# Performance work log

Measured on AMD Instinct MI355X. Metric: run time of the kernel, lower is better.

The kernel has to match this reference:

```python
import jax, jax.numpy as jnp
import numpy as np

EPS = 1e-10

def _iou(a, b):
    """IoU for boxes in (cx, cy, w, h) format; a, b: (..., 4)."""
    a_min = a[..., :2] - a[..., 2:] * 0.5
    a_max = a[..., :2] + a[..., 2:] * 0.5
    b_min = b[..., :2] - b[..., 2:] * 0.5
    b_max = b[..., :2] + b[..., 2:] * 0.5
    inter_wh = jnp.clip(jnp.minimum(a_max, b_max) - jnp.maximum(a_min, b_min), 0.0)
    inter = inter_wh[..., 0] * inter_wh[..., 1]
    area_a = a[..., 2] * a[..., 3]
    area_b = b[..., 2] * b[..., 3]
    return inter / (area_a + area_b - inter + EPS)

def setup_inputs() -> dict:
    key = jax.random.key(0)
    k1, k2, k3 = jax.random.split(key, 3)
    BATCH, S, C = 16384, 7, 30
    # uniform in (0.01, 1) so sqrt() of w,h channels is finite/differentiable
    preds = jax.random.uniform(k1, (BATCH, S, S, C), jnp.float32, 0.01, 1.0)
    labels = jax.random.uniform(k2, (BATCH, S, S, C), jnp.float32, 0.01, 1.0)
    obj = jax.random.bernoulli(k3, 0.15, (BATCH, S, S)).astype(jnp.float32)
    labels = labels.at[..., 4].set(obj)  # code branches on labels[...,4] == 1
    return {"preds": preds, "labels": labels}

def reference(preds, labels):
    batch = preds.shape[0]
    obj = labels[..., 4] == 1.0  # (B, S, S)
    # faithful quirk: label bbox x-coord is read transposed (labels[i, y, x, 0])
    lb0 = jnp.swapaxes(labels[..., 0], 1, 2)
    lbox = jnp.stack([lb0, labels[..., 1], labels[..., 2], labels[..., 3]], axis=-1)
    iou1 = _iou(preds[..., 0:4], lbox)
    iou2 = _iou(preds[..., 5:9], lbox)
    choose1 = iou1 > iou2
    # branch where box 1 is responsible
    b1 = (5.0 * jnp.sum((preds[..., 0:2] - labels[..., 0:2]) ** 2, -1)
          + jnp.sum((jnp.sqrt(preds[..., 2:4]) - jnp.sqrt(labels[..., 2:4])) ** 2, -1)
          + (iou1 - preds[..., 4]) ** 2
          + 0.5 * preds[..., 9] ** 2)
    # branch where box 2 is responsible (targets read from labels[...,5:9] as in source)
    b2 = (5.0 * jnp.sum((preds[..., 5:7] - labels[..., 5:7]) ** 2, -1)
          + jnp.sum((jnp.sqrt(preds[..., 7:9]) - jnp.sqrt(labels[..., 7:9])) ** 2, -1)
          + (iou2 - preds[..., 9]) ** 2
          + 0.5 * preds[..., 4] ** 2)
    cls = jnp.sum((labels[..., 10:] - preds[..., 10:]) ** 2, -1)
    obj_loss = jnp.where(choose1, b1, b2) + cls
    noobj_loss = 0.5 * (preds[..., 4] ** 2 + preds[..., 9] ** 2)
    total = jnp.sum(jnp.where(obj, obj_loss, noobj_loss))
    return total / batch
```

## Files before the change

### kernel.cpp

```cpp
#include <hip/hip_runtime.h>


#define BATCH 16384
#define S 7
#define C 30
#define NCELLS (BATCH * S * S)
#define BLOCK 256
#define NC 256
#define NBLK (NCELLS / NC)
#define F4_PER_ARR (NC * C / 4)

typedef float f4v __attribute__((ext_vector_type(4)));

__device__ __forceinline__ f4v ntld(const f4v* p) {
    return __builtin_nontemporal_load(p);
}

__device__ __forceinline__ float sq(float v) { return v * v; }

__device__ __forceinline__ float iou_box(float acx, float acy, float aw, float ah,
                                         float bcx, float bcy, float bw, float bh) {
    float ax0 = acx - aw * 0.5f, ax1 = acx + aw * 0.5f;
    float ay0 = acy - ah * 0.5f, ay1 = acy + ah * 0.5f;
    float bx0 = bcx - bw * 0.5f, bx1 = bcx + bw * 0.5f;
    float by0 = bcy - bh * 0.5f, by1 = bcy + bh * 0.5f;
    float iw = fmaxf(fminf(ax1, bx1) - fmaxf(ax0, bx0), 0.0f);
    float ih = fmaxf(fminf(ay1, by1) - fmaxf(ay0, by0), 0.0f);
    float inter = iw * ih;
    float denom = aw * ah + bw * bh - inter + 1e-10f;
    return inter / denom;
}

__global__ __launch_bounds__(BLOCK) void yolo_partial_kernel(
        const float* __restrict__ preds,
        const float* __restrict__ labels,
        float* __restrict__ partials) {
    __shared__ __align__(16) float sp[NC * C];
    __shared__ __align__(16) float sl[NC * C];

    const int tid  = threadIdx.x;
    const int lane = tid & 63;
    const int wv   = tid >> 6;
    const int base_cell = blockIdx.x * NC;

    const f4v* gp = reinterpret_cast<const f4v*>(preds  + (size_t)base_cell * C);
    const f4v* gl = reinterpret_cast<const f4v*>(labels + (size_t)base_cell * C);
    f4v* s4l = reinterpret_cast<f4v*>(sl);
    f4v* s4p = reinterpret_cast<f4v*>(sp);

    f4v rl[8], rp[8];
    #pragma unroll
    for (int k = 0; k < 7; ++k) rl[k] = ntld(gl + tid + k * BLOCK);
    #pragma unroll
    for (int k = 0; k < 7; ++k) rp[k] = ntld(gp + tid + k * BLOCK);
    const int tl = 1792 + (tid & 127);
    if (tid < 128) rl[7] = ntld(gl + tl);
    else           rp[7] = ntld(gp + tl);

    #pragma unroll
    for (int k = 0; k < 7; ++k) s4l[tid + k * BLOCK] = rl[k];
    #pragma unroll
    for (int k = 0; k < 7; ++k) s4p[tid + k * BLOCK] = rp[k];
    if (tid < 128) s4l[tl] = rl[7];
    else           s4p[tl] = rp[7];
    __syncthreads();

    const float* p = sp + tid * C;
    const float* l = sl + tid * C;
    float pv[C], lv[C];
    #pragma unroll
    for (int i = 0; i < C / 2; ++i) {
        float2 tp = *reinterpret_cast<const float2*>(p + 2 * i);
        pv[2 * i] = tp.x; pv[2 * i + 1] = tp.y;
        float2 tl2 = *reinterpret_cast<const float2*>(l + 2 * i);
        lv[2 * i] = tl2.x; lv[2 * i + 1] = tl2.y;
    }

    int cell = base_cell + tid;
    int b    = cell / (S * S);
    int rem  = cell - b * (S * S);
    int y    = rem / S;
    int x    = rem - y * S;
    int pc   = b * (S * S) + x * S + y;
    float lb0;
    if (pc >= base_cell && pc < base_cell + NC) {
        lb0 = sl[(pc - base_cell) * C];
    } else {
        lb0 = labels[(size_t)pc * C];
    }

    float iou1 = iou_box(pv[0], pv[1], pv[2], pv[3], lb0, lv[1], lv[2], lv[3]);
    float iou2 = iou_box(pv[5], pv[6], pv[7], pv[8], lb0, lv[1], lv[2], lv[3]);

    float b1 = 5.0f * (sq(pv[0] - lv[0]) + sq(pv[1] - lv[1]))
             + sq(sqrtf(pv[2]) - sqrtf(lv[2])) + sq(sqrtf(pv[3]) - sqrtf(lv[3]))
             + sq(iou1 - pv[4])
             + 0.5f * pv[9] * pv[9];

    float b2 = 5.0f * (sq(pv[5] - lv[5]) + sq(pv[6] - lv[6]))
             + sq(sqrtf(pv[7]) - sqrtf(lv[7])) + sq(sqrtf(pv[8]) - sqrtf(lv[8]))
             + sq(iou2 - pv[9])
             + 0.5f * pv[4] * pv[4];

    float cls = 0.0f;
    #pragma unroll
    for (int c = 10; c < C; ++c) cls += sq(lv[c] - pv[c]);

    float obj_loss   = ((iou1 > iou2) ? b1 : b2) + cls;
    float noobj_loss = 0.5f * (pv[4] * pv[4] + pv[9] * pv[9]);
    float loss = (lv[4] == 1.0f) ? obj_loss : noobj_loss;

    #pragma unroll
    for (int off = 32; off > 0; off >>= 1)
        loss += __shfl_down(loss, off, 64);

    __shared__ float wsum[BLOCK / 64];
    if (lane == 0) wsum[wv] = loss;
    __syncthreads();
    if (tid == 0) {
        partials[blockIdx.x] = wsum[0] + wsum[1] + wsum[2] + wsum[3];
    }
}

__global__ __launch_bounds__(BLOCK) void yolo_reduce_kernel(
        const float* __restrict__ partials,
        float* __restrict__ out) {
    const int tid = threadIdx.x;
    float s = 0.0f;
    for (int i = tid; i < NBLK; i += BLOCK) s += partials[i];

    #pragma unroll
    for (int off = 32; off > 0; off >>= 1)
        s += __shfl_down(s, off, 64);

    __shared__ float wsum[BLOCK / 64];
    int lane = tid & 63;
    int wv   = tid >> 6;
    if (lane == 0) wsum[wv] = s;
    __syncthreads();
    if (tid == 0) {
        out[0] = (wsum[0] + wsum[1] + wsum[2] + wsum[3]) * (1.0f / (float)BATCH);
    }
}

extern "C" void kernel_launch(void* const* d_in, const int* in_sizes, int n_in,
                              void* d_out, int out_size, void* d_ws, size_t ws_size,
                              hipStream_t stream) {
    const float* preds  = (const float*)d_in[0];
    const float* labels = (const float*)d_in[1];
    float* out = (float*)d_out;
    float* partials = (float*)d_ws;

    yolo_partial_kernel<<<NBLK, BLOCK, 0, stream>>>(preds, labels, partials);
    yolo_reduce_kernel<<<1, BLOCK, 0, stream>>>(partials, out);
}
```

Measured before the change: 197.0 us.

## Process two cell groups per block, prefetching the second into registers during compute

```diff
diff --git a/kernel.cpp b/kernel.cpp
--- a/kernel.cpp
+++ b/kernel.cpp
@@ -7,8 +7,8 @@
 #define NCELLS (BATCH * S * S)
 #define BLOCK 256
 #define NC 256
-#define NBLK (NCELLS / NC)
-#define F4_PER_ARR (NC * C / 4)
+#define NGRP (NCELLS / NC)
+#define NBLK2 (NGRP / 2)
 
 typedef float f4v __attribute__((ext_vector_type(4)));
 
@@ -31,40 +31,36 @@
     return inter / denom;
 }
 
-__global__ __launch_bounds__(BLOCK) void yolo_partial_kernel(
-        const float* __restrict__ preds,
-        const float* __restrict__ labels,
-        float* __restrict__ partials) {
-    __shared__ __align__(16) float sp[NC * C];
-    __shared__ __align__(16) float sl[NC * C];
-
-    const int tid  = threadIdx.x;
-    const int lane = tid & 63;
-    const int wv   = tid >> 6;
-    const int base_cell = blockIdx.x * NC;
-
+__device__ __forceinline__ void stage_regs(const float* __restrict__ preds,
+                                           const float* __restrict__ labels,
+                                           int base_cell, int tid, int tl,
+                                           f4v* rp, f4v* rl) {
     const f4v* gp = reinterpret_cast<const f4v*>(preds  + (size_t)base_cell * C);
     const f4v* gl = reinterpret_cast<const f4v*>(labels + (size_t)base_cell * C);
-    f4v* s4l = reinterpret_cast<f4v*>(sl);
-    f4v* s4p = reinterpret_cast<f4v*>(sp);
-
-    f4v rl[8], rp[8];
     #pragma unroll
     for (int k = 0; k < 7; ++k) rl[k] = ntld(gl + tid + k * BLOCK);
     #pragma unroll
     for (int k = 0; k < 7; ++k) rp[k] = ntld(gp + tid + k * BLOCK);
-    const int tl = 1792 + (tid & 127);
     if (tid < 128) rl[7] = ntld(gl + tl);
     else           rp[7] = ntld(gp + tl);
+}
 
+__device__ __forceinline__ void write_lds(float* sp, float* sl, int tid, int tl,
+                                          const f4v* rp, const f4v* rl) {
+    f4v* s4l = reinterpret_cast<f4v*>(sl);
+    f4v* s4p = reinterpret_cast<f4v*>(sp);
     #pragma unroll
     for (int k = 0; k < 7; ++k) s4l[tid + k * BLOCK] = rl[k];
     #pragma unroll
     for (int k = 0; k < 7; ++k) s4p[tid + k * BLOCK] = rp[k];
     if (tid < 128) s4l[tl] = rl[7];
     else           s4p[tl] = rp[7];
-    __syncthreads();
+}
 
+__device__ __forceinline__ float cell_loss(const float* __restrict__ sp,
+                                           const float* __restrict__ sl,
+                                           const float* __restrict__ labels,
+                                           int base_cell, int tid) {
     const float* p = sp + tid * C;
     const float* l = sl + tid * C;
     float pv[C], lv[C];
@@ -108,18 +104,52 @@
 
     float obj_loss   = ((iou1 > iou2) ? b1 : b2) + cls;
     float noobj_loss = 0.5f * (pv[4] * pv[4] + pv[9] * pv[9]);
-    float loss = (lv[4] == 1.0f) ? obj_loss : noobj_loss;
+    return (lv[4] == 1.0f) ? obj_loss : noobj_loss;
+}
 
+__global__ __launch_bounds__(BLOCK) void yolo_partial_kernel(
+        const float* __restrict__ preds,
+        const float* __restrict__ labels,
+        float* __restrict__ partials) {
+    __shared__ __align__(16) float sp[NC * C];
+    __shared__ __align__(16) float sl[NC * C];
+    __shared__ float wsum[BLOCK / 64];
+
+    const int tid  = threadIdx.x;
+    const int lane = tid & 63;
+    const int wv   = tid >> 6;
+    const int tl   = 1792 + (tid & 127);
+    const int g0   = blockIdx.x * 2;
+    const int g1   = g0 + 1;
+
+    f4v rl[8], rp[8];
+
+    stage_regs(preds, labels, g0 * NC, tid, tl, rp, rl);
+    write_lds(sp, sl, tid, tl, rp, rl);
+    __syncthreads();
+
+    stage_regs(preds, labels, g1 * NC, tid, tl, rp, rl);
+
+    float loss = cell_loss(sp, sl, labels, g0 * NC, tid);
     #pragma unroll
     for (int off = 32; off > 0; off >>= 1)
         loss += __shfl_down(loss, off, 64);
-
-    __shared__ float wsum[BLOCK / 64];
     if (lane == 0) wsum[wv] = loss;
     __syncthreads();
-    if (tid == 0) {
-        partials[blockIdx.x] = wsum[0] + wsum[1] + wsum[2] + wsum[3];
-    }
+    if (tid == 0)
+        partials[g0] = wsum[0] + wsum[1] + wsum[2] + wsum[3];
+
+    write_lds(sp, sl, tid, tl, rp, rl);
+    __syncthreads();
+
+    loss = cell_loss(sp, sl, labels, g1 * NC, tid);
+    #pragma unroll
+    for (int off = 32; off > 0; off >>= 1)
+        loss += __shfl_down(loss, off, 64);
+    if (lane == 0) wsum[wv] = loss;
+    __syncthreads();
+    if (tid == 0)
+        partials[g1] = wsum[0] + wsum[1] + wsum[2] + wsum[3];
 }
 
 __global__ __launch_bounds__(BLOCK) void yolo_reduce_kernel(
@@ -127,7 +157,7 @@
         float* __restrict__ out) {
     const int tid = threadIdx.x;
     float s = 0.0f;
-    for (int i = tid; i < NBLK; i += BLOCK) s += partials[i];
+    for (int i = tid; i < NGRP; i += BLOCK) s += partials[i];
 
     #pragma unroll
     for (int off = 32; off > 0; off >>= 1)
@@ -151,6 +181,6 @@
     float* out = (float*)d_out;
     float* partials = (float*)d_ws;
 
-    yolo_partial_kernel<<<NBLK, BLOCK, 0, stream>>>(preds, labels, partials);
+    yolo_partial_kernel<<<NBLK2, BLOCK, 0, stream>>>(preds, labels, partials);
     yolo_reduce_kernel<<<1, BLOCK, 0, stream>>>(partials, out);
 }
```

New measurement: 198.6 us. About the same (+0.8%).
